# Kernel optimization log

Measured on AMD Instinct MI355X. Metric: run time of the kernel, lower is better.

## Reference

```python
import jax, jax.numpy as jnp
import numpy as np

UNITS = 1000


def gru_step(x, h, W, U, b):
    # Keras GRU, reset_after=True. b: [2, 3*units] = (input bias, recurrent bias)
    gx = x @ W + b[0]
    gh = h @ U + b[1]
    xz, xr, xh = jnp.split(gx, 3, axis=-1)
    hz, hr, hh_ = jnp.split(gh, 3, axis=-1)
    z = jax.nn.sigmoid(xz + hz)
    r = jax.nn.sigmoid(xr + hr)
    hh = jnp.tanh(xh + r * hh_)
    return z * h + (1.0 - z) * hh


def setup_inputs() -> dict:
    key = jax.random.key(0)
    ks = jax.random.split(key, 12)
    V1, E, U = 32001, 100, UNITS
    B, S = 64, 25
    sc = 0.05
    return {
        "x": jax.random.randint(ks[0], (B, S), 0, V1, dtype=jnp.int32),
        "target": jax.random.randint(ks[1], (B, S), 0, V1, dtype=jnp.int32),
        "start_token": 2,
        "emb_table": jax.random.normal(ks[2], (V1, E), jnp.float32) * sc,
        "enc_kernel": jax.random.normal(ks[3], (E, 3 * U), jnp.float32) * sc,
        "enc_recurrent": jax.random.normal(ks[4], (U, 3 * U), jnp.float32) * sc,
        "enc_bias": jax.random.normal(ks[5], (2, 3 * U), jnp.float32) * sc,
        "dec_kernel": jax.random.normal(ks[6], (E, 3 * U), jnp.float32) * sc,
        "dec_recurrent": jax.random.normal(ks[7], (U, 3 * U), jnp.float32) * sc,
        "dec_bias": jax.random.normal(ks[8], (2, 3 * U), jnp.float32) * sc,
        "fc_w": jax.random.normal(ks[9], (U, V1), jnp.float32) * sc,
        "fc_b": jnp.zeros((V1,), jnp.float32),
    }


def reference(x, target, start_token, emb_table, enc_kernel, enc_recurrent,
              enc_bias, dec_kernel, dec_recurrent, dec_bias, fc_w, fc_b):
    B, S = x.shape
    max_len = target.shape[1]

    # ---- Encoder (computed faithfully; its output is unused downstream,
    # matching the original where attention is never invoked) ----
    emb_x = emb_table[x]                      # [B,S,E]
    mask_x = (x != 0)                          # mask_zero embedding

    def enc_scan(h, xm):
        xt, mt = xm                            # xt:[B,E], mt:[B]
        hn = gru_step(xt, h, enc_kernel, enc_recurrent, enc_bias)
        h = jnp.where(mt[:, None], hn, h)      # masked steps carry state
        return h, h

    h0 = jnp.zeros((B, UNITS), emb_x.dtype)
    enc_state, enc_out = jax.lax.scan(
        enc_scan, h0, (jnp.swapaxes(emb_x, 0, 1), jnp.swapaxes(mask_x, 0, 1)))

    # ---- Decoder: original calls gru WITHOUT initial_state, so every step
    # starts from a zero hidden state -> all timesteps are independent. ----
    # teacher-forced inputs: [start_token, target[:, :-1]]
    tokens = jnp.concatenate(
        [jnp.full((B, 1), start_token, dtype=target.dtype), target[:, :-1]], axis=1)  # [B,T]
    emb_d = emb_table[tokens]                  # [B,T,E]
    mask_d = (tokens != 0)                     # [B,T]

    h_zero = jnp.zeros((B, max_len, UNITS), emb_d.dtype)
    h1 = gru_step(emb_d, h_zero, dec_kernel, dec_recurrent, dec_bias)  # [B,T,U]
    # masked single step -> output is the zero initial output
    h1 = jnp.where(mask_d[..., None], h1, 0.0)

    logits = h1 @ fc_w + fc_b                  # [B,T,V+1]
    app_emb = logits.astype(jnp.float32) @ emb_table  # [B,T,E]
    return app_emb
```

## Files before the change

### kernel.cpp

```cpp
#include <hip/hip_runtime.h>

typedef _Float16 half_t;
typedef _Float16 half8 __attribute__((ext_vector_type(8)));
typedef float    floatx4 __attribute__((ext_vector_type(4)));

#define V1     32001
#define EMBD   100
#define UNITS  1000
#define SEQ    25
#define NROWS  1600
#define KPAD   32032
#define HSTR   1024
#define NKB    36
#define KUQ    28
#define PROWS  1024

__global__ __launch_bounds__(256) void kPre(
    const float* __restrict__ E, half_t* __restrict__ ET,
    const float* __restrict__ fcb, float* __restrict__ vvec,
    const int* __restrict__ target, const int* __restrict__ stok,
    const float* __restrict__ K, const float* __restrict__ bias,
    half_t* __restrict__ h1h)
{
    __shared__ char smem[100 * 66 * sizeof(half_t)];
    const int tid = threadIdx.x;
    const int bid = blockIdx.x;

    if (bid < 501) {
        half_t* lds = (half_t*)smem;
        const int k0 = bid * 64;
        const int e  = tid & 127;
        const int kh = tid >> 7;
        for (int kk = kh; kk < 64; kk += 2) {
            const int k = k0 + kk;
            float v = 0.f;
            if (k < 32000 && e < 100) v = E[k * 100 + e];
            if (e < 100) lds[e * 66 + kk] = (half_t)v;
        }
        __syncthreads();
        const int kl = tid & 63;
        const int eh = tid >> 6;
        if (k0 + kl < KPAD) {
            for (int ee = eh; ee < 100; ee += 4)
                ET[(long)ee * KPAD + k0 + kl] = lds[ee * 66 + kl];
        }
        return;
    }

    if (bid < 757) {
        const int e  = tid & 127;
        const int g  = tid >> 7;
        const int ec = min(e, 99);
        const int slice = (bid - 501) * 2 + g;
        const int chunk = (V1 + 511) / 512;
        const int j0 = slice * chunk;
        const int j1 = min(j0 + chunk, V1);
        float acc = 0.f;
        for (int j = j0; j < j1; ++j)
            acc += fcb[j] * E[j * 100 + ec];
        if (e < 100) atomicAdd(&vvec[e], acc);
        return;
    }

    float (*xs)[100] = (float(*)[100])smem;
    __shared__ int msk[8];
    const int b3    = bid - 757;
    const int rg    = b3 % 200;
    const int uc    = b3 / 200;
    const int ibase = rg * 8;
    {
        const int r = tid >> 5, c = tid & 31;
        const int i = ibase + r;
        const int bb = i / SEQ, t = i - bb * SEQ;
        const int token = (t == 0) ? stok[0] : target[bb * SEQ + t - 1];
        if (c == 0) msk[r] = (token != 0);
        for (int cc = c; cc < 100; cc += 32)
            xs[r][cc] = E[token * 100 + cc];
    }
    __syncthreads();

    const int u = uc * 256 + tid;
    if (u < UNITS) {
        float az[8], ar[8], ah[8];
#pragma unroll
        for (int r = 0; r < 8; ++r) { az[r] = 0.f; ar[r] = 0.f; ah[r] = 0.f; }
#pragma unroll 4
        for (int k = 0; k < 100; ++k) {
            const float wz = K[k * 3000 + u];
            const float wr = K[k * 3000 + 1000 + u];
            const float wh = K[k * 3000 + 2000 + u];
#pragma unroll
            for (int r = 0; r < 8; ++r) {
                const float x = xs[r][k];
                az[r] += x * wz;
                ar[r] += x * wr;
                ah[r] += x * wh;
            }
        }
        const float* b0 = bias;
        const float* b1 = bias + 3000;
        const float bz  = b0[u] + b1[u];
        const float br  = b0[1000 + u] + b1[1000 + u];
        const float bh0 = b0[2000 + u];
        const float bh1 = b1[2000 + u];
#pragma unroll
        for (int r = 0; r < 8; ++r) {
            const float z   = 1.f / (1.f + __expf(-(az[r] + bz)));
            const float rg_ = 1.f / (1.f + __expf(-(ar[r] + br)));
            const float pre = ah[r] + bh0 + rg_ * bh1;
            const float ex  = __expf(2.f * pre);
            const float hh  = 1.f - 2.f / (ex + 1.f);
            h1h[(ibase + r) * HSTR + u] = (half_t)(msk[r] ? (1.f - z) * hh : 0.f);
        }
    } else {
        const half_t cv = (half_t)((u == 1000) ? 1.f : 0.f);
#pragma unroll
        for (int r = 0; r < 8; ++r)
            h1h[(ibase + r) * HSTR + u] = cv;
    }
}

__global__ __launch_bounds__(256) void kA(const float* __restrict__ W,
                                          const half_t* __restrict__ ET,
                                          float* __restrict__ P)
{
    const int tid   = threadIdx.x;
    const int lane  = tid & 63;
    const int wv    = tid >> 6;
    const int mgrp  = blockIdx.x;
    const int kq    = blockIdx.y;
    const int row16 = lane & 15;
    const int quad  = lane >> 4;

    const int m  = mgrp * 64 + wv * 16 + row16;
    const int mc = min(m, UNITS - 1);
    const float* wrow = W + (long)mc * V1;

    const int wb = kq * KUQ;
    const int we = min(wb + KUQ, 1000);

    floatx4 acc[7];
#pragma unroll
    for (int t = 0; t < 7; ++t) acc[t] = (floatx4){0.f, 0.f, 0.f, 0.f};

    const half_t* bb[7];
#pragma unroll
    for (int t = 0; t < 7; ++t) {
        const int nc = min(t * 16 + row16, 99);
        bb[t] = ET + (long)nc * KPAD + quad * 8;
    }

    int un = wb;
    for (; un + 4 <= we; un += 4) {
        float fa[4][8];
        half8 vb[4][7];
#pragma unroll
        for (int j = 0; j < 4; ++j) {
            const int k0 = (un + j) * 32 + quad * 8;
            __builtin_memcpy(&fa[j][0], wrow + k0, 32);
        }
#pragma unroll
        for (int j = 0; j < 4; ++j) {
            const int koff = (un + j) * 32;
#pragma unroll
            for (int t = 0; t < 7; ++t)
                vb[j][t] = *(const half8*)(bb[t] + koff);
        }
#pragma unroll
        for (int j = 0; j < 4; ++j) {
            half8 a;
#pragma unroll
            for (int q = 0; q < 8; ++q) a[q] = (half_t)fa[j][q];
#pragma unroll
            for (int t = 0; t < 7; ++t)
                acc[t] = __builtin_amdgcn_mfma_f32_16x16x32_f16(a, vb[j][t], acc[t], 0, 0, 0);
        }
    }
    for (; un < we; ++un) {
        const int k0 = un * 32 + quad * 8;
        float f0[8];
        __builtin_memcpy(f0, wrow + k0, 32);
        half8 a;
#pragma unroll
        for (int q = 0; q < 8; ++q) a[q] = (half_t)f0[q];
#pragma unroll
        for (int t = 0; t < 7; ++t) {
            const half8 b = *(const half8*)(bb[t] + un * 32);
            acc[t] = __builtin_amdgcn_mfma_f32_16x16x32_f16(a, b, acc[t], 0, 0, 0);
        }
    }

    float* Pk = P + (long)kq * (PROWS * 100);
    const int orow0 = mgrp * 64 + wv * 16 + quad * 4;
#pragma unroll
    for (int t = 0; t < 7; ++t) {
        const int col = t * 16 + row16;
        if (col < 100) {
#pragma unroll
            for (int r = 0; r < 4; ++r)
                Pk[(orow0 + r) * 100 + col] = acc[t][r];
        }
    }
}

__global__ __launch_bounds__(256) void kPost(const float* __restrict__ P,
                                             const float* __restrict__ W,
                                             const float* __restrict__ E,
                                             const float* __restrict__ vvec,
                                             half_t* __restrict__ MbT)
{
    const int idx = blockIdx.x * 256 + threadIdx.x;
    const int kk  = idx / 100;
    const int e   = idx - kk * 100;
    float s;
    if (kk < 1000) {
        s = 0.f;
#pragma unroll 4
        for (int kb = 0; kb < NKB; ++kb)
            s += P[(long)kb * (PROWS * 100) + kk * 100 + e];
        s += W[(long)kk * V1 + 32000] * E[32000 * 100 + e];
    } else if (kk == 1000) {
        s = vvec[e];
    } else {
        s = 0.f;
    }
    MbT[e * HSTR + kk] = (half_t)s;
}

__global__ __launch_bounds__(256) void kC(const half_t* __restrict__ h1h,
                                          const half_t* __restrict__ MbT,
                                          float* __restrict__ out)
{
    __shared__ float red[3][64][29];
    const int tid   = threadIdx.x;
    const int lane  = tid & 63;
    const int wv    = tid >> 6;
    const int rb    = blockIdx.x;
    const int row16 = lane & 15;
    const int quad  = lane >> 4;

    const half_t* arow = h1h + (long)(rb * 16 + row16) * HSTR + quad * 8;
    const half_t* bbase[7];
#pragma unroll
    for (int t = 0; t < 7; ++t) {
        const int nc = min(t * 16 + row16, 99);
        bbase[t] = MbT + (long)nc * HSTR + quad * 8;
    }

    floatx4 acc[7];
#pragma unroll
    for (int t = 0; t < 7; ++t) acc[t] = (floatx4){0.f, 0.f, 0.f, 0.f};

    const int wb = wv * 8;
#pragma unroll 2
    for (int un = wb; un < wb + 8; ++un) {
        const half8 a = *(const half8*)(arow + un * 32);
#pragma unroll
        for (int t = 0; t < 7; ++t) {
            const half8 b = *(const half8*)(bbase[t] + un * 32);
            acc[t] = __builtin_amdgcn_mfma_f32_16x16x32_f16(a, b, acc[t], 0, 0, 0);
        }
    }

    if (wv > 0) {
#pragma unroll
        for (int t = 0; t < 7; ++t)
#pragma unroll
            for (int r = 0; r < 4; ++r)
                red[wv - 1][lane][t * 4 + r] = acc[t][r];
    }
    __syncthreads();
    if (wv == 0) {
        const int orow0 = rb * 16 + quad * 4;
#pragma unroll
        for (int t = 0; t < 7; ++t) {
            const int col = t * 16 + row16;
            if (col < 100) {
#pragma unroll
                for (int r = 0; r < 4; ++r) {
                    const int i = t * 4 + r;
                    out[(orow0 + r) * 100 + col] = acc[t][r] + red[0][lane][i]
                        + red[1][lane][i] + red[2][lane][i];
                }
            }
        }
    }
}

extern "C" void kernel_launch(void* const* d_in, const int* in_sizes, int n_in,
                              void* d_out, int out_size, void* d_ws, size_t ws_size,
                              hipStream_t stream)
{
    const int*   target     = (const int*)d_in[1];
    const int*   start_tok  = (const int*)d_in[2];
    const float* emb        = (const float*)d_in[3];
    const float* dec_kernel = (const float*)d_in[7];
    const float* dec_bias   = (const float*)d_in[9];
    const float* fc_w       = (const float*)d_in[10];
    const float* fc_b       = (const float*)d_in[11];

    float*  vvec = (float*)d_ws;
    half_t* ET   = (half_t*)(vvec + 128);
    half_t* h1h  = ET + (size_t)100 * KPAD;
    half_t* MbT  = h1h + (size_t)NROWS * HSTR;
    float*  P    = (float*)(MbT + (size_t)100 * HSTR);
    float*  out  = (float*)d_out;

    hipMemsetAsync(vvec, 0, 128 * sizeof(float), stream);

    kPre<<<1557, 256, 0, stream>>>(emb, ET, fc_b, vvec, target, start_tok,
                                   dec_kernel, dec_bias, h1h);
    kA<<<dim3(16, NKB), 256, 0, stream>>>(fc_w, ET, P);
    kPost<<<(PROWS * 100) / 256, 256, 0, stream>>>(P, fc_w, emb, vvec, MbT);
    kC<<<100, 256, 0, stream>>>(h1h, MbT, out);
}
```

Measured before the change: 348.5 us.

## Stage embedding tiles in LDS with double buffering and split-K in final GEMM

Result: faster. 298.0 us (-14.5%).

```diff
diff --git a/kernel.cpp b/kernel.cpp
--- a/kernel.cpp
+++ b/kernel.cpp
@@ -9,14 +9,14 @@
 #define UNITS  1000
 #define SEQ    25
 #define NROWS  1600
-#define KPAD   32032
 #define HSTR   1024
-#define NKB    36
-#define KUQ    28
-#define PROWS  1024
+#define NKB    63
+#define UPQ    16
+#define BROWS  128
+#define BSTR   40
 
 __global__ __launch_bounds__(256) void kPre(
-    const float* __restrict__ E, half_t* __restrict__ ET,
+    const float* __restrict__ E, half_t* __restrict__ ETu,
     const float* __restrict__ fcb, float* __restrict__ vvec,
     const int* __restrict__ target, const int* __restrict__ stok,
     const float* __restrict__ K, const float* __restrict__ bias,
@@ -26,32 +26,31 @@
     const int tid = threadIdx.x;
     const int bid = blockIdx.x;
 
-    if (bid < 501) {
+    if (bid < 500) {
         half_t* lds = (half_t*)smem;
         const int k0 = bid * 64;
         const int e  = tid & 127;
         const int kh = tid >> 7;
         for (int kk = kh; kk < 64; kk += 2) {
             const int k = k0 + kk;
-            float v = 0.f;
-            if (k < 32000 && e < 100) v = E[k * 100 + e];
-            if (e < 100) lds[e * 66 + kk] = (half_t)v;
+            if (e < 100) lds[e * 66 + kk] = (half_t)E[k * 100 + e];
         }
         __syncthreads();
-        const int kl = tid & 63;
-        const int eh = tid >> 6;
-        if (k0 + kl < KPAD) {
-            for (int ee = eh; ee < 100; ee += 4)
-                ET[(long)ee * KPAD + k0 + kl] = lds[ee * 66 + kl];
-        }
+        const int kl   = tid & 63;
+        const int eh   = tid >> 6;
+        const int unit = (k0 + kl) >> 5;
+        const int kc   = kl & 31;
+        half_t* dst = ETu + (long)unit * (BROWS * 32) + kc;
+        for (int ee = eh; ee < BROWS; ee += 4)
+            dst[ee * 32] = (ee < 100) ? lds[ee * 66 + kl] : (half_t)0.f;
         return;
     }
 
-    if (bid < 757) {
+    if (bid < 756) {
         const int e  = tid & 127;
         const int g  = tid >> 7;
         const int ec = min(e, 99);
-        const int slice = (bid - 501) * 2 + g;
+        const int slice = (bid - 500) * 2 + g;
         const int chunk = (V1 + 511) / 512;
         const int j0 = slice * chunk;
         const int j1 = min(j0 + chunk, V1);
@@ -64,7 +63,7 @@
 
     float (*xs)[100] = (float(*)[100])smem;
     __shared__ int msk[8];
-    const int b3    = bid - 757;
+    const int b3    = bid - 756;
     const int rg    = b3 % 200;
     const int uc    = b3 / 200;
     const int ibase = rg * 8;
@@ -121,9 +120,10 @@
 }
 
 __global__ __launch_bounds__(256) void kA(const float* __restrict__ W,
-                                          const half_t* __restrict__ ET,
-                                          float* __restrict__ P)
-{
+                                          const half_t* __restrict__ ETu,
+                                          half_t* __restrict__ P)
+{
+    __shared__ half_t Bs[2][BROWS * BSTR];
     const int tid   = threadIdx.x;
     const int lane  = tid & 63;
     const int wv    = tid >> 6;
@@ -132,65 +132,51 @@
     const int row16 = lane & 15;
     const int quad  = lane >> 4;
 
+    const int ub = kq * UPQ;
+    const int nu = min(UPQ, UNITS - ub);
+
     const int m  = mgrp * 64 + wv * 16 + row16;
     const int mc = min(m, UNITS - 1);
     const float* wrow = W + (long)mc * V1;
 
-    const int wb = kq * KUQ;
-    const int we = min(wb + KUQ, 1000);
+    const int srow  = tid >> 2;
+    const int scol  = (tid & 3) * 8;
+    const int soff0 = srow * BSTR + scol;
+    const int soff1 = (64 + srow) * BSTR + scol;
+    const int goff0 = tid * 8;
+    const int goff1 = 2048 + tid * 8;
 
     floatx4 acc[7];
 #pragma unroll
     for (int t = 0; t < 7; ++t) acc[t] = (floatx4){0.f, 0.f, 0.f, 0.f};
 
-    const half_t* bb[7];
-#pragma unroll
-    for (int t = 0; t < 7; ++t) {
-        const int nc = min(t * 16 + row16, 99);
-        bb[t] = ET + (long)nc * KPAD + quad * 8;
-    }
-
-    int un = wb;
-    for (; un + 4 <= we; un += 4) {
-        float fa[4][8];
-        half8 vb[4][7];
-#pragma unroll
-        for (int j = 0; j < 4; ++j) {
-            const int k0 = (un + j) * 32 + quad * 8;
-            __builtin_memcpy(&fa[j][0], wrow + k0, 32);
-        }
-#pragma unroll
-        for (int j = 0; j < 4; ++j) {
-            const int koff = (un + j) * 32;
-#pragma unroll
-            for (int t = 0; t < 7; ++t)
-                vb[j][t] = *(const half8*)(bb[t] + koff);
-        }
-#pragma unroll
-        for (int j = 0; j < 4; ++j) {
-            half8 a;
-#pragma unroll
-            for (int q = 0; q < 8; ++q) a[q] = (half_t)fa[j][q];
-#pragma unroll
-            for (int t = 0; t < 7; ++t)
-                acc[t] = __builtin_amdgcn_mfma_f32_16x16x32_f16(a, vb[j][t], acc[t], 0, 0, 0);
-        }
-    }
-    for (; un < we; ++un) {
-        const int k0 = un * 32 + quad * 8;
-        float f0[8];
-        __builtin_memcpy(f0, wrow + k0, 32);
+    half8 rb0 = *(const half8*)(ETu + (long)ub * (BROWS * 32) + goff0);
+    half8 rb1 = *(const half8*)(ETu + (long)ub * (BROWS * 32) + goff1);
+    float fa[8];
+    __builtin_memcpy(fa, wrow + ub * 32 + quad * 8, 32);
+
+    for (int i = 0; i < nu; ++i) {
+        *(half8*)(&Bs[i & 1][soff0]) = rb0;
+        *(half8*)(&Bs[i & 1][soff1]) = rb1;
         half8 a;
 #pragma unroll
-        for (int q = 0; q < 8; ++q) a[q] = (half_t)f0[q];
+        for (int q = 0; q < 8; ++q) a[q] = (half_t)fa[q];
+        if (i + 1 < nu) {
+            const long nt = (long)(ub + i + 1) * (BROWS * 32);
+            rb0 = *(const half8*)(ETu + nt + goff0);
+            rb1 = *(const half8*)(ETu + nt + goff1);
+            __builtin_memcpy(fa, wrow + (ub + i + 1) * 32 + quad * 8, 32);
+        }
+        __syncthreads();
+        const half_t* bp = &Bs[i & 1][row16 * BSTR + quad * 8];
 #pragma unroll
         for (int t = 0; t < 7; ++t) {
-            const half8 b = *(const half8*)(bb[t] + un * 32);
+            const half8 b = *(const half8*)(bp + t * 16 * BSTR);
             acc[t] = __builtin_amdgcn_mfma_f32_16x16x32_f16(a, b, acc[t], 0, 0, 0);
         }
     }
 
-    float* Pk = P + (long)kq * (PROWS * 100);
+    half_t* Pk = P + (long)kq * (1024 * 100);
     const int orow0 = mgrp * 64 + wv * 16 + quad * 4;
 #pragma unroll
     for (int t = 0; t < 7; ++t) {
@@ -198,12 +184,12 @@
         if (col < 100) {
 #pragma unroll
             for (int r = 0; r < 4; ++r)
-                Pk[(orow0 + r) * 100 + col] = acc[t][r];
-        }
-    }
-}
-
-__global__ __launch_bounds__(256) void kPost(const float* __restrict__ P,
+                Pk[(orow0 + r) * 100 + col] = (half_t)acc[t][r];
+        }
+    }
+}
+
+__global__ __launch_bounds__(256) void kPost(const half_t* __restrict__ P,
                                              const float* __restrict__ W,
                                              const float* __restrict__ E,
                                              const float* __restrict__ vvec,
@@ -215,9 +201,9 @@
     float s;
     if (kk < 1000) {
         s = 0.f;
-#pragma unroll 4
+#pragma unroll 9
         for (int kb = 0; kb < NKB; ++kb)
-            s += P[(long)kb * (PROWS * 100) + kk * 100 + e];
+            s += (float)P[(long)kb * (1024 * 100) + kk * 100 + e];
         s += W[(long)kk * V1 + 32000] * E[32000 * 100 + e];
     } else if (kk == 1000) {
         s = vvec[e];
@@ -236,6 +222,7 @@
     const int lane  = tid & 63;
     const int wv    = tid >> 6;
     const int rb    = blockIdx.x;
+    const int ks    = blockIdx.y;
     const int row16 = lane & 15;
     const int quad  = lane >> 4;
 
@@ -251,9 +238,9 @@
 #pragma unroll
     for (int t = 0; t < 7; ++t) acc[t] = (floatx4){0.f, 0.f, 0.f, 0.f};
 
-    const int wb = wv * 8;
-#pragma unroll 2
-    for (int un = wb; un < wb + 8; ++un) {
+    const int wb = ks * 8 + wv * 2;
+#pragma unroll
+    for (int un = wb; un < wb + 2; ++un) {
         const half8 a = *(const half8*)(arow + un * 32);
 #pragma unroll
         for (int t = 0; t < 7; ++t) {
@@ -279,8 +266,9 @@
 #pragma unroll
                 for (int r = 0; r < 4; ++r) {
                     const int i = t * 4 + r;
-                    out[(orow0 + r) * 100 + col] = acc[t][r] + red[0][lane][i]
-                        + red[1][lane][i] + red[2][lane][i];
+                    const float s = acc[t][r] + red[0][lane][i]
+                                  + red[1][lane][i] + red[2][lane][i];
+                    atomicAdd(&out[(orow0 + r) * 100 + col], s);
                 }
             }
         }
@@ -300,17 +288,18 @@
     const float* fc_b       = (const float*)d_in[11];
 
     float*  vvec = (float*)d_ws;
-    half_t* ET   = (half_t*)(vvec + 128);
-    half_t* h1h  = ET + (size_t)100 * KPAD;
+    half_t* ETu  = (half_t*)(vvec + 128);
+    half_t* h1h  = ETu + (size_t)UNITS * (BROWS * 32);
     half_t* MbT  = h1h + (size_t)NROWS * HSTR;
-    float*  P    = (float*)(MbT + (size_t)100 * HSTR);
+    half_t* P    = MbT + (size_t)100 * HSTR;
     float*  out  = (float*)d_out;
 
     hipMemsetAsync(vvec, 0, 128 * sizeof(float), stream);
-
-    kPre<<<1557, 256, 0, stream>>>(emb, ET, fc_b, vvec, target, start_tok,
+    hipMemsetAsync(out, 0, (size_t)NROWS * EMBD * sizeof(float), stream);
+
+    kPre<<<1556, 256, 0, stream>>>(emb, ETu, fc_b, vvec, target, start_tok,
                                    dec_kernel, dec_bias, h1h);
-    kA<<<dim3(16, NKB), 256, 0, stream>>>(fc_w, ET, P);
-    kPost<<<(PROWS * 100) / 256, 256, 0, stream>>>(P, fc_w, emb, vvec, MbT);
-    kC<<<100, 256, 0, stream>>>(h1h, MbT, out);
-}
+    kA<<<dim3(16, NKB), 256, 0, stream>>>(fc_w, ETu, P);
+    kPost<<<(1024 * 100) / 256, 256, 0, stream>>>(P, fc_w, emb, vvec, MbT);
+    kC<<<dim3(100, 4), 256, 0, stream>>>(h1h, MbT, out);
+}
```
